# Performance work log

Hardware: AMD Instinct MI355X
Metric: run time of the kernel (lower is better)

## Reference

```python
import math
import jax, jax.numpy as jnp
import numpy as np

H, D = 16, 128
INNER = H * D
QUERY_DIM = 2048
EPS = 1e-6
NUM_SEQ_SHIFTS = 16
MAX_SEQ_LEN = 2048
CHANNEL_SHIFTS = [1, 2, 4, 8]


def compute_seq_shifts(num_shifts, max_len=2048):
    if num_shifts <= 1:
        return [0]
    half = (num_shifts - 1 + 1) // 2
    max_s = max(max_len // 2, 2)
    if half <= 1:
        positive = [1]
    else:
        positive = sorted(set(max(1, round(math.exp(math.log(max_s) * i / (half - 1)))) for i in range(half)))
        while len(positive) < half:
            new_vals = []
            for i in range(len(positive) - 1):
                mid = (positive[i] + positive[i + 1]) // 2
                if mid not in positive and mid not in new_vals:
                    new_vals.append(mid)
                if len(positive) + len(new_vals) >= half:
                    break
            if not new_vals:
                v = positive[-1] + 1
                while len(positive) + len(new_vals) < half and v <= max_s:
                    new_vals.append(v)
                    v += 1
            positive = sorted(set(positive + new_vals))[:half]
    shifts = [0]
    for s in positive:
        shifts.append(s)
        shifts.append(-s)
    return shifts[:num_shifts]

SEQ_SHIFTS = compute_seq_shifts(NUM_SEQ_SHIFTS, MAX_SEQ_LEN)


def setup_inputs() -> dict:
    key = jax.random.key(0)
    ks = jax.random.split(key, 12)
    s = 0.02
    return {
        "x": jax.random.normal(ks[0], (2, 2048, QUERY_DIM), dtype=jnp.float32),
        "wq": jax.random.normal(ks[1], (INNER, QUERY_DIM), dtype=jnp.float32) * s,
        "bq": jnp.zeros((INNER,), jnp.float32),
        "wk": jax.random.normal(ks[2], (INNER, QUERY_DIM), dtype=jnp.float32) * s,
        "bk": jnp.zeros((INNER,), jnp.float32),
        "wv": jax.random.normal(ks[3], (INNER, QUERY_DIM), dtype=jnp.float32) * s,
        "bv": jnp.zeros((INNER,), jnp.float32),
        "gq": jnp.ones((INNER,), jnp.float32),
        "gk": jnp.ones((INNER,), jnp.float32),
        "w_mix": jax.random.normal(ks[4], (1, 1 + len(CHANNEL_SHIFTS)), dtype=jnp.float32) * 0.4,
        "wo": jax.random.normal(ks[5], (QUERY_DIM, INNER), dtype=jnp.float32) * s,
        "bo": jnp.zeros((QUERY_DIM,), jnp.float32),
    }


def _rmsnorm(x, g, eps=EPS):
    return x * jax.lax.rsqrt(jnp.mean(x * x, axis=-1, keepdims=True) + eps) * g


def reference(x, wq, bq, wk, bk, wv, bv, gq, gk, w_mix, wo, bo):
    B, L, _ = x.shape
    scale = D ** (-0.5)
    q = _rmsnorm(x @ wq.T + bq, gq).reshape(B, L, H, D)
    k = _rmsnorm(x @ wk.T + bk, gk).reshape(B, L, H, D)
    v = (x @ wv.T + bv).reshape(B, L, H, D)
    # rolled gather indices: roll(k, s, axis=1)[l] == k[(l - s) % L]
    shifts = np.asarray(SEQ_SHIFTS)  # [S]
    idx = (np.arange(L)[None, :] - shifts[:, None]) % L  # [S, L]
    k_sh = k[:, idx]  # [B, S, L, H, D]
    v_sh = v[:, idx]  # [B, S, L, H, D]
    # channel-shifted q variants: [base, roll 1, 2, 4, 8] along D
    q_all = jnp.stack([q] + [jnp.roll(q, c, axis=-1) for c in CHANNEL_SHIFTS], axis=0)  # [C, B, L, H, D]
    scores = jnp.einsum('cblhd,bslhd->blhsc', q_all, k_sh) * scale  # [B, L, H, S, C]
    mixed = jnp.einsum('blhsc,c->blhs', scores, w_mix[0])  # score_mix Linear(C,1,bias=False)
    attn = jax.nn.softmax(mixed, axis=-1)  # softmax over shifts
    out = jnp.einsum('blhs,bslhd->blhd', attn, v_sh).reshape(B, L, H * D)
    return out @ wo.T + bo
```

## Files before the change

### kernel.cpp

```cpp
#include <hip/hip_runtime.h>
#include <hip/hip_bf16.h>
#include <stdint.h>

typedef __attribute__((ext_vector_type(8))) short v8s;
typedef __attribute__((ext_vector_type(8))) __bf16 bf16x8;
typedef __attribute__((ext_vector_type(4))) float v4f;

__device__ __forceinline__ unsigned short f2bf(float f) {
  unsigned int u = __float_as_uint(f);
  u += 0x7fff + ((u >> 16) & 1);
  return (unsigned short)(u >> 16);
}
__device__ __forceinline__ float bf2f(unsigned short h) {
  return __uint_as_float(((unsigned int)h) << 16);
}

__device__ __forceinline__ void gload_lds16(const void* g, void* l) {
  __builtin_amdgcn_global_load_lds(
      (const __attribute__((address_space(1))) void*)g,
      (__attribute__((address_space(3))) void*)l,
      16, 0, 0);
}

__global__ void cast_main(const float* __restrict__ x,  const float* __restrict__ wq,
                          const float* __restrict__ wk, const float* __restrict__ wv,
                          const float* __restrict__ wo,
                          unsigned short* __restrict__ xb, unsigned short* __restrict__ wqkvb,
                          unsigned short* __restrict__ wob) {
  const size_t MK = 8388608, NK = 4194304;
  size_t i = ((size_t)blockIdx.x * 256 + threadIdx.x) * 4;
  const float* s; unsigned short* d; size_t off;
  if (i < MK)               { s = x;  d = xb;              off = i; }
  else if (i < MK + NK)     { s = wq; d = wqkvb;           off = i - MK; }
  else if (i < MK + 2 * NK) { s = wk; d = wqkvb + NK;      off = i - MK - NK; }
  else if (i < MK + 3 * NK) { s = wv; d = wqkvb + 2 * NK;  off = i - MK - 2 * NK; }
  else                      { s = wo; d = wob;             off = i - MK - 3 * NK; }
  float4 v = *(const float4*)(s + off);
  ushort4 o;
  o.x = f2bf(v.x); o.y = f2bf(v.y); o.z = f2bf(v.z); o.w = f2bf(v.w);
  *(ushort4*)(d + off) = o;
}

#define BM 128
#define BN 128
#define BK 64

template <int OUT>
__global__ __launch_bounds__(256, 2) void gemm_bt(
    const unsigned short* __restrict__ A,
    const unsigned short* __restrict__ B,
    const float* __restrict__ bias0,
    const float* __restrict__ bias1,
    const float* __restrict__ bias2,
    void* __restrict__ D0, void* __restrict__ D1, void* __restrict__ D2,
    int K)
{
  __shared__ __align__(16) unsigned short Sh[2 * BM * BK];
  unsigned short* As = Sh;
  unsigned short* Bs = Sh + BM * BK;

  const int tid  = threadIdx.x;
  const int lane = tid & 63;
  const int wid  = tid >> 6;
  const int wr   = wid >> 1, wc = wid & 1;

  const int tm = blockIdx.y * BM;
  const int tn = blockIdx.x * BN;

  const int srow = lane >> 3;
  const int scb  = lane & 7;
  const int gco  = (scb ^ srow) * 8;

  v4f acc[4][4];
#pragma unroll
  for (int m = 0; m < 4; ++m)
#pragma unroll
    for (int n = 0; n < 4; ++n)
      acc[m][n] = (v4f){0.f, 0.f, 0.f, 0.f};

  const unsigned short* Ab = A + (size_t)tm * K;
  const unsigned short* Bb = B + (size_t)tn * K;
  const int kTiles = K / BK;

  for (int kt = 0; kt < kTiles; ++kt) {
    const int k0 = kt * BK;
#pragma unroll
    for (int i = 0; i < 4; ++i) {
      const int r0 = wid * 32 + i * 8;
      gload_lds16(Ab + (size_t)(r0 + srow) * K + k0 + gco, &As[r0 * BK]);
    }
#pragma unroll
    for (int i = 0; i < 4; ++i) {
      const int r0 = wid * 32 + i * 8;
      gload_lds16(Bb + (size_t)(r0 + srow) * K + k0 + gco, &Bs[r0 * BK]);
    }
    __syncthreads();

#pragma unroll
    for (int ks = 0; ks < 2; ++ks) {
      bf16x8 av[4], bv[4];
#pragma unroll
      for (int m = 0; m < 4; ++m) {
        const int row  = wr * 64 + m * 16 + (lane & 15);
        const int cl   = ks * 4 + (lane >> 4);
        av[m] = *(const bf16x8*)&As[row * BK + ((cl ^ (row & 7)) * 8)];
      }
#pragma unroll
      for (int n = 0; n < 4; ++n) {
        const int row  = wc * 64 + n * 16 + (lane & 15);
        const int cl   = ks * 4 + (lane >> 4);
        bv[n] = *(const bf16x8*)&Bs[row * BK + ((cl ^ (row & 7)) * 8)];
      }
#pragma unroll
      for (int m = 0; m < 4; ++m)
#pragma unroll
        for (int n = 0; n < 4; ++n)
          acc[m][n] = __builtin_amdgcn_mfma_f32_16x16x32_bf16(av[m], bv[n], acc[m][n], 0, 0, 0);
    }
    __syncthreads();
  }

  const int cr0 = tm + wr * 64 + (lane >> 4) * 4;
  const int cc0 = tn + wc * 64 + (lane & 15);

  if (OUT == 0) {
    float* Dp = (float*)D0;
#pragma unroll
    for (int n = 0; n < 4; ++n) {
      const int col = cc0 + n * 16;
      const float bz = bias0[col];
#pragma unroll
      for (int m = 0; m < 4; ++m) {
#pragma unroll
        for (int r = 0; r < 4; ++r) {
          const int rr = cr0 + m * 16 + r;
          Dp[(size_t)rr * 2048 + col] = acc[m][n][r] + bz;
        }
      }
    }
  } else {
    const int sid = tn >> 11;
    const float* bp = (sid == 0) ? bias0 : (sid == 1) ? bias1 : bias2;
    unsigned short* Dq = (unsigned short*)((sid == 0) ? D0 : (sid == 1) ? D1 : D2);

    const int rl0 = wr * 64 + (lane >> 4) * 4;
    const int clb = wc * 64 + (lane & 15);
#pragma unroll
    for (int n = 0; n < 4; ++n) {
      const int cl = clb + n * 16;
      const float bz = bp[(tn & 2047) + cl];
#pragma unroll
      for (int m = 0; m < 4; ++m) {
#pragma unroll
        for (int r = 0; r < 4; ++r) {
          Sh[(rl0 + m * 16 + r) * 128 + cl] = f2bf(acc[m][n][r] + bz);
        }
      }
    }
    __syncthreads();

    if (sid < 2) {
      const int tn2 = tn & 2047;
#pragma unroll
      for (int it = 0; it < 8; ++it) {
        const int off = (it * 256 + tid) * 8;
        const int row = off >> 7, col = off & 127;
        *(v8s*)(Dq + (size_t)(tm + row) * 2048 + tn2 + col) = *(const v8s*)&Sh[off];
      }
    } else {
      const int bb = tm >> 11, ll0 = tm & 2047;
      const int hh = (tn & 2047) >> 7;
      unsigned short* dst = Dq + (((size_t)(bb * 16 + hh)) * 2048 + ll0) * 128;
#pragma unroll
      for (int it = 0; it < 8; ++it) {
        const int off = (it * 256 + tid) * 8;
        *(v8s*)(dst + off) = *(const v8s*)&Sh[off];
      }
    }
  }
}

__global__ __launch_bounds__(256) void rmsnorm_mix(
    const unsigned short* __restrict__ Qb, const unsigned short* __restrict__ Kb,
    unsigned short* __restrict__ Qt, unsigned short* __restrict__ Kt,
    const float* __restrict__ gq, const float* __restrict__ gk,
    const float* __restrict__ wmix)
{
  const int row = blockIdx.x;
  const bool isQ = (blockIdx.y == 0);
  const unsigned short* src = (isQ ? Qb : Kb) + (size_t)row * 2048;
  unsigned short* dstbase = isQ ? Qt : Kt;
  const float* g = isQ ? gq : gk;
  const int b = row >> 11, l = row & 2047;

  __shared__ float sv[2048];
  __shared__ float red[4];

  const int t = threadIdx.x;
  v8s raw = *(const v8s*)(src + t * 8);
  float x[8];
  float ss = 0.f;
#pragma unroll
  for (int j = 0; j < 8; ++j) { x[j] = bf2f((unsigned short)raw[j]); ss += x[j] * x[j]; }
#pragma unroll
  for (int o = 32; o > 0; o >>= 1) ss += __shfl_xor(ss, o, 64);
  if ((t & 63) == 0) red[t >> 6] = ss;
  __syncthreads();
  const float tot = red[0] + red[1] + red[2] + red[3];
  const float inv = rsqrtf(tot * (1.0f / 2048.0f) + 1e-6f);

  const int h = t >> 4;
  unsigned short* dst = dstbase + (((size_t)(b * 16 + h)) * 2048 + l) * 128 + ((t * 8) & 127);

  if (isQ) {
#pragma unroll
    for (int j = 0; j < 8; ++j) sv[t * 8 + j] = x[j] * inv * g[t * 8 + j];
    __syncthreads();
    const float scale = 0.08838834764831845f;
    const float w0 = wmix[0], w1 = wmix[1], w2 = wmix[2], w3 = wmix[3], w4 = wmix[4];
    v8s ov;
#pragma unroll
    for (int j = 0; j < 8; ++j) {
      const int idx = t * 8 + j;
      const int hb = idx & ~127;
      const int d  = idx & 127;
      float a = w0 * sv[hb + d]
              + w1 * sv[hb + ((d - 1) & 127)]
              + w2 * sv[hb + ((d - 2) & 127)]
              + w3 * sv[hb + ((d - 4) & 127)]
              + w4 * sv[hb + ((d - 8) & 127)];
      ov[j] = (short)f2bf(a * scale);
    }
    *(v8s*)dst = ov;
  } else {
    v8s ov;
#pragma unroll
    for (int j = 0; j < 8; ++j) ov[j] = (short)f2bf(x[j] * inv * g[t * 8 + j]);
    *(v8s*)dst = ov;
  }
}

__global__ __launch_bounds__(512, 1) void attention_k(
    const unsigned short* __restrict__ Qt,
    const unsigned short* __restrict__ Kt,
    const unsigned short* __restrict__ Vt,
    unsigned short* __restrict__ AO)
{
  const int bid   = blockIdx.x;
  const int plane = bid & 31;
  const int ch    = bid >> 5;
  const int b = plane >> 4, h = plane & 15;
  const int l0 = ch * 128;
  const int w0 = (l0 + 2048 - 64) & 2047;

  __shared__ __align__(16) unsigned short Ks[256 * 128];
  __shared__ __align__(16) unsigned short Vs[256 * 128];
  __shared__ float sc[128][17];

  const int t    = threadIdx.x;
  const int lane = t & 63;
  const int w    = t >> 6;
  const int li   = t >> 2;
  const int q    = t & 3;
  const int myl  = l0 + li;

  const size_t pbase = (size_t)plane * (2048 * 128);

  {
    const int lr4 = lane >> 4;
    const int cp  = lane & 15;
#pragma unroll
    for (int j = 0; j < 8; ++j) {
      const int seg = w * 8 + j;
      const int rl  = seg * 4 + lr4;
      const int cl  = cp ^ (rl & 7);
      const int g   = (w0 + rl) & 2047;
      gload_lds16(Kt + pbase + (size_t)g * 128 + cl * 8, &Ks[seg * 512]);
      gload_lds16(Vt + pbase + (size_t)g * 128 + cl * 8, &Vs[seg * 512]);
    }
  }

  float qf[32];
  {
    const unsigned short* qp = Qt + pbase + (size_t)myl * 128 + q * 32;
#pragma unroll
    for (int i = 0; i < 4; ++i) {
      v8s qv = *(const v8s*)(qp + i * 8);
#pragma unroll
      for (int j = 0; j < 8; ++j) qf[i * 8 + j] = bf2f((unsigned short)qv[j]);
    }
  }

  asm volatile("s_waitcnt vmcnt(0)" ::: "memory");
  __syncthreads();

  const int SH[16] = {0, 1, -1, 3, -3, 7, -7, 20, -20, 53, -53, 141, -141, 380, -380, 1024};

#pragma unroll
  for (int s = 0; s < 16; ++s) {
    float dot = 0.f;
    if (s < 11) {
      const int rl = li + 64 - SH[s];
#pragma unroll
      for (int i = 0; i < 4; ++i) {
        v8s kv = *(const v8s*)&Ks[rl * 128 + (((q * 4 + i) ^ (rl & 7)) * 8)];
#pragma unroll
        for (int j = 0; j < 8; ++j) dot += qf[i * 8 + j] * bf2f((unsigned short)kv[j]);
      }
    } else {
      const int row = (myl - SH[s]) & 2047;
      const unsigned short* kp = Kt + pbase + (size_t)row * 128 + q * 32;
#pragma unroll
      for (int i = 0; i < 4; ++i) {
        v8s kv = *(const v8s*)(kp + i * 8);
#pragma unroll
        for (int j = 0; j < 8; ++j) dot += qf[i * 8 + j] * bf2f((unsigned short)kv[j]);
      }
    }
    dot += __shfl_xor(dot, 1, 64);
    dot += __shfl_xor(dot, 2, 64);
    if (q == 0) sc[li][s] = dot;
  }
  __syncthreads();

  {
    float v0[16];
#pragma unroll
    for (int s = 0; s < 16; ++s) v0[s] = sc[li][s];
    float mx = v0[0];
#pragma unroll
    for (int s = 1; s < 16; ++s) mx = fmaxf(mx, v0[s]);
    float sum = 0.f;
    float e[4];
#pragma unroll
    for (int s = 0; s < 16; ++s) {
      const float ee = __expf(v0[s] - mx);
      sum += ee;
      if ((s >> 2) == q) e[s & 3] = ee;
    }
    const float inv = 1.f / sum;
    __syncthreads();
#pragma unroll
    for (int i = 0; i < 4; ++i) sc[li][q * 4 + i] = e[i] * inv;
  }
  __syncthreads();

  float o[32];
#pragma unroll
  for (int i = 0; i < 32; ++i) o[i] = 0.f;
#pragma unroll
  for (int s = 0; s < 16; ++s) {
    const float p = sc[li][s];
    if (s < 11) {
      const int rl = li + 64 - SH[s];
#pragma unroll
      for (int i = 0; i < 4; ++i) {
        v8s vv = *(const v8s*)&Vs[rl * 128 + (((q * 4 + i) ^ (rl & 7)) * 8)];
#pragma unroll
        for (int j = 0; j < 8; ++j) o[i * 8 + j] += p * bf2f((unsigned short)vv[j]);
      }
    } else {
      const int row = (myl - SH[s]) & 2047;
      const unsigned short* vp = Vt + pbase + (size_t)row * 128 + q * 32;
#pragma unroll
      for (int i = 0; i < 4; ++i) {
        v8s vv = *(const v8s*)(vp + i * 8);
#pragma unroll
        for (int j = 0; j < 8; ++j) o[i * 8 + j] += p * bf2f((unsigned short)vv[j]);
      }
    }
  }

  unsigned short* op = AO + ((size_t)(b * 2048 + myl)) * 2048 + h * 128 + q * 32;
#pragma unroll
  for (int i = 0; i < 4; ++i) {
    v8s ov;
#pragma unroll
    for (int j = 0; j < 8; ++j) ov[j] = (short)f2bf(o[i * 8 + j]);
    *(v8s*)(op + i * 8) = ov;
  }
}

extern "C" void kernel_launch(void* const* d_in, const int* in_sizes, int n_in,
                              void* d_out, int out_size, void* d_ws, size_t ws_size,
                              hipStream_t stream) {
  const float* x    = (const float*)d_in[0];
  const float* wq   = (const float*)d_in[1];
  const float* bq   = (const float*)d_in[2];
  const float* wk   = (const float*)d_in[3];
  const float* bk   = (const float*)d_in[4];
  const float* wv   = (const float*)d_in[5];
  const float* bv   = (const float*)d_in[6];
  const float* gq   = (const float*)d_in[7];
  const float* gk   = (const float*)d_in[8];
  const float* wmix = (const float*)d_in[9];
  const float* wo   = (const float*)d_in[10];
  const float* bo   = (const float*)d_in[11];

  const int M = 4096;
  const int K = 2048;
  const size_t MB = 1024 * 1024;

  char* ws = (char*)d_ws;
  unsigned short* xb    = (unsigned short*)(ws + 0 * MB);
  unsigned short* Ktr   = (unsigned short*)(ws + 0 * MB);
  unsigned short* wqkvb = (unsigned short*)(ws + 16 * MB);
  unsigned short* Qb    = (unsigned short*)(ws + 40 * MB);
  unsigned short* AOb   = (unsigned short*)(ws + 40 * MB);
  unsigned short* Kb    = (unsigned short*)(ws + 56 * MB);
  unsigned short* Vt    = (unsigned short*)(ws + 72 * MB);
  unsigned short* Qtr   = (unsigned short*)(ws + 88 * MB);
  unsigned short* wob   = (unsigned short*)(ws + 104 * MB);

  cast_main<<<24576, 256, 0, stream>>>(x, wq, wk, wv, wo, xb, wqkvb, wob);

  gemm_bt<1><<<dim3(48, 32), 256, 0, stream>>>(xb, wqkvb, bq, bk, bv, Qb, Kb, Vt, K);

  rmsnorm_mix<<<dim3(M, 2), 256, 0, stream>>>(Qb, Kb, Qtr, Ktr, gq, gk, wmix);
  attention_k<<<512, 512, 0, stream>>>(Qtr, Ktr, Vt, AOb);

  gemm_bt<0><<<dim3(16, 32), 256, 0, stream>>>(AOb, wob, bo, nullptr, nullptr, d_out, nullptr, nullptr, K);
}
```

Before: 222.1 us.

## Fold RMSNorm scaling and channel mix into attention, keep only row norms

The separate normalize-and-transpose pass over Q and K is replaced by a small kernel that only computes the inverse RMS per row. The attention kernel now reads raw Q/K in row-major layout, applies the norm, gains and channel-shift mix to Q in registers (using a lane shuffle for wraparound), and scales each score by the key's inverse norm. This drops a full write and reread of normalized Q/K tensors. In exchange K loads become strided across rows of width 2048, and there are extra per-score loads of invK.

```diff
diff --git a/kernel.cpp b/kernel.cpp
--- a/kernel.cpp
+++ b/kernel.cpp
@@ -180,70 +180,37 @@
   }
 }
 
-__global__ __launch_bounds__(256) void rmsnorm_mix(
+__global__ __launch_bounds__(256) void row_norms(
     const unsigned short* __restrict__ Qb, const unsigned short* __restrict__ Kb,
-    unsigned short* __restrict__ Qt, unsigned short* __restrict__ Kt,
-    const float* __restrict__ gq, const float* __restrict__ gk,
-    const float* __restrict__ wmix)
+    float* __restrict__ invQ, float* __restrict__ invK)
 {
   const int row = blockIdx.x;
   const bool isQ = (blockIdx.y == 0);
   const unsigned short* src = (isQ ? Qb : Kb) + (size_t)row * 2048;
-  unsigned short* dstbase = isQ ? Qt : Kt;
-  const float* g = isQ ? gq : gk;
-  const int b = row >> 11, l = row & 2047;
-
-  __shared__ float sv[2048];
   __shared__ float red[4];
 
   const int t = threadIdx.x;
   v8s raw = *(const v8s*)(src + t * 8);
-  float x[8];
   float ss = 0.f;
 #pragma unroll
-  for (int j = 0; j < 8; ++j) { x[j] = bf2f((unsigned short)raw[j]); ss += x[j] * x[j]; }
+  for (int j = 0; j < 8; ++j) { float x = bf2f((unsigned short)raw[j]); ss += x * x; }
 #pragma unroll
   for (int o = 32; o > 0; o >>= 1) ss += __shfl_xor(ss, o, 64);
   if ((t & 63) == 0) red[t >> 6] = ss;
   __syncthreads();
-  const float tot = red[0] + red[1] + red[2] + red[3];
-  const float inv = rsqrtf(tot * (1.0f / 2048.0f) + 1e-6f);
-
-  const int h = t >> 4;
-  unsigned short* dst = dstbase + (((size_t)(b * 16 + h)) * 2048 + l) * 128 + ((t * 8) & 127);
-
-  if (isQ) {
-#pragma unroll
-    for (int j = 0; j < 8; ++j) sv[t * 8 + j] = x[j] * inv * g[t * 8 + j];
-    __syncthreads();
-    const float scale = 0.08838834764831845f;
-    const float w0 = wmix[0], w1 = wmix[1], w2 = wmix[2], w3 = wmix[3], w4 = wmix[4];
-    v8s ov;
-#pragma unroll
-    for (int j = 0; j < 8; ++j) {
-      const int idx = t * 8 + j;
-      const int hb = idx & ~127;
-      const int d  = idx & 127;
-      float a = w0 * sv[hb + d]
-              + w1 * sv[hb + ((d - 1) & 127)]
-              + w2 * sv[hb + ((d - 2) & 127)]
-              + w3 * sv[hb + ((d - 4) & 127)]
-              + w4 * sv[hb + ((d - 8) & 127)];
-      ov[j] = (short)f2bf(a * scale);
-    }
-    *(v8s*)dst = ov;
-  } else {
-    v8s ov;
-#pragma unroll
-    for (int j = 0; j < 8; ++j) ov[j] = (short)f2bf(x[j] * inv * g[t * 8 + j]);
-    *(v8s*)dst = ov;
+  if (t == 0) {
+    const float tot = red[0] + red[1] + red[2] + red[3];
+    (isQ ? invQ : invK)[row] = rsqrtf(tot * (1.0f / 2048.0f) + 1e-6f);
   }
 }
 
 __global__ __launch_bounds__(512, 1) void attention_k(
-    const unsigned short* __restrict__ Qt,
-    const unsigned short* __restrict__ Kt,
+    const unsigned short* __restrict__ Qb,
+    const unsigned short* __restrict__ Kb,
     const unsigned short* __restrict__ Vt,
+    const float* __restrict__ invQ, const float* __restrict__ invK,
+    const float* __restrict__ gq, const float* __restrict__ gk,
+    const float* __restrict__ wmix,
     unsigned short* __restrict__ AO)
 {
   const int bid   = blockIdx.x;
@@ -263,6 +230,7 @@
   const int li   = t >> 2;
   const int q    = t & 3;
   const int myl  = l0 + li;
+  const int grow = b * 2048 + myl;
 
   const size_t pbase = (size_t)plane * (2048 * 128);
 
@@ -275,19 +243,39 @@
       const int rl  = seg * 4 + lr4;
       const int cl  = cp ^ (rl & 7);
       const int g   = (w0 + rl) & 2047;
-      gload_lds16(Kt + pbase + (size_t)g * 128 + cl * 8, &Ks[seg * 512]);
+      gload_lds16(Kb + ((size_t)(b * 2048 + g)) * 2048 + h * 128 + cl * 8, &Ks[seg * 512]);
       gload_lds16(Vt + pbase + (size_t)g * 128 + cl * 8, &Vs[seg * 512]);
     }
   }
 
-  float qf[32];
+  float qg[32];
   {
-    const unsigned short* qp = Qt + pbase + (size_t)myl * 128 + q * 32;
+    float qn[32];
+    const unsigned short* qp = Qb + (size_t)grow * 2048 + h * 128 + q * 32;
+    const float iq = invQ[grow];
+    const float* gqp = gq + h * 128 + q * 32;
 #pragma unroll
     for (int i = 0; i < 4; ++i) {
       v8s qv = *(const v8s*)(qp + i * 8);
 #pragma unroll
-      for (int j = 0; j < 8; ++j) qf[i * 8 + j] = bf2f((unsigned short)qv[j]);
+      for (int j = 0; j < 8; ++j)
+        qn[i * 8 + j] = bf2f((unsigned short)qv[j]) * iq * gqp[i * 8 + j];
+    }
+    float prev[8];
+    const int nb = (t & ~3) | ((q + 3) & 3);
+#pragma unroll
+    for (int j = 0; j < 8; ++j) prev[j] = __shfl(qn[24 + j], nb & 63, 64);
+    const float scale = 0.08838834764831845f;
+    const float w0m = wmix[0] * scale, w1m = wmix[1] * scale, w2m = wmix[2] * scale;
+    const float w3m = wmix[3] * scale, w4m = wmix[4] * scale;
+    const float* gkp = gk + h * 128 + q * 32;
+#pragma unroll
+    for (int i = 0; i < 32; ++i) {
+      const float s1 = (i >= 1) ? qn[i - 1] : prev[7 + i];
+      const float s2 = (i >= 2) ? qn[i - 2] : prev[6 + i];
+      const float s4 = (i >= 4) ? qn[i - 4] : prev[4 + i];
+      const float s8 = (i >= 8) ? qn[i - 8] : prev[i];
+      qg[i] = (w0m * qn[i] + w1m * s1 + w2m * s2 + w3m * s4 + w4m * s8) * gkp[i];
     }
   }
 
@@ -298,6 +286,7 @@
 
 #pragma unroll
   for (int s = 0; s < 16; ++s) {
+    const int row = (myl - SH[s]) & 2047;
     float dot = 0.f;
     if (s < 11) {
       const int rl = li + 64 - SH[s];
@@ -305,21 +294,20 @@
       for (int i = 0; i < 4; ++i) {
         v8s kv = *(const v8s*)&Ks[rl * 128 + (((q * 4 + i) ^ (rl & 7)) * 8)];
 #pragma unroll
-        for (int j = 0; j < 8; ++j) dot += qf[i * 8 + j] * bf2f((unsigned short)kv[j]);
+        for (int j = 0; j < 8; ++j) dot += qg[i * 8 + j] * bf2f((unsigned short)kv[j]);
       }
     } else {
-      const int row = (myl - SH[s]) & 2047;
-      const unsigned short* kp = Kt + pbase + (size_t)row * 128 + q * 32;
+      const unsigned short* kp = Kb + ((size_t)(b * 2048 + row)) * 2048 + h * 128 + q * 32;
 #pragma unroll
       for (int i = 0; i < 4; ++i) {
         v8s kv = *(const v8s*)(kp + i * 8);
 #pragma unroll
-        for (int j = 0; j < 8; ++j) dot += qf[i * 8 + j] * bf2f((unsigned short)kv[j]);
+        for (int j = 0; j < 8; ++j) dot += qg[i * 8 + j] * bf2f((unsigned short)kv[j]);
       }
     }
     dot += __shfl_xor(dot, 1, 64);
     dot += __shfl_xor(dot, 2, 64);
-    if (q == 0) sc[li][s] = dot;
+    if (q == 0) sc[li][s] = dot * invK[b * 2048 + row];
   }
   __syncthreads();
 
@@ -371,7 +359,7 @@
     }
   }
 
-  unsigned short* op = AO + ((size_t)(b * 2048 + myl)) * 2048 + h * 128 + q * 32;
+  unsigned short* op = AO + ((size_t)grow) * 2048 + h * 128 + q * 32;
 #pragma unroll
   for (int i = 0; i < 4; ++i) {
     v8s ov;
@@ -403,21 +391,22 @@
 
   char* ws = (char*)d_ws;
   unsigned short* xb    = (unsigned short*)(ws + 0 * MB);
-  unsigned short* Ktr   = (unsigned short*)(ws + 0 * MB);
   unsigned short* wqkvb = (unsigned short*)(ws + 16 * MB);
+  unsigned short* AOb   = (unsigned short*)(ws + 16 * MB);
+  float*          invQ  = (float*)(ws + 33 * MB);
+  float*          invK  = (float*)(ws + 33 * MB + 16384);
   unsigned short* Qb    = (unsigned short*)(ws + 40 * MB);
-  unsigned short* AOb   = (unsigned short*)(ws + 40 * MB);
   unsigned short* Kb    = (unsigned short*)(ws + 56 * MB);
   unsigned short* Vt    = (unsigned short*)(ws + 72 * MB);
-  unsigned short* Qtr   = (unsigned short*)(ws + 88 * MB);
   unsigned short* wob   = (unsigned short*)(ws + 104 * MB);
 
   cast_main<<<24576, 256, 0, stream>>>(x, wq, wk, wv, wo, xb, wqkvb, wob);
 
   gemm_bt<1><<<dim3(48, 32), 256, 0, stream>>>(xb, wqkvb, bq, bk, bv, Qb, Kb, Vt, K);
 
-  rmsnorm_mix<<<dim3(M, 2), 256, 0, stream>>>(Qb, Kb, Qtr, Ktr, gq, gk, wmix);
-  attention_k<<<512, 512, 0, stream>>>(Qtr, Ktr, Vt, AOb);
+  row_norms<<<dim3(M, 2), 256, 0, stream>>>(Qb, Kb, invQ, invK);
+
+  attention_k<<<512, 512, 0, stream>>>(Qb, Kb, Vt, invQ, invK, gq, gk, wmix, AOb);
 
   gemm_bt<0><<<dim3(16, 32), 256, 0, stream>>>(AOb, wob, bo, nullptr, nullptr, d_out, nullptr, nullptr, K);
 }
```

Result: faster. 215.6 us (-2.9%).
